# Optimization experiments

Measured on AMD Instinct MI355X. Metric: run time of the kernel, lower is better.

## Reference

```python
import jax, jax.numpy as jnp
import numpy as np

B, T, D = 4, 2048, 1024
DK, DV = 1024, 1024
BETA1, BETA2 = 1.0, 1.0
EPS = 1e-12  # torch F.normalize eps


def setup_inputs() -> dict:
    key = jax.random.key(0)
    kx, kq, kk, kv, ko = jax.random.split(key, 5)
    def w(k, shape):
        return jax.random.normal(k, shape, dtype=jnp.float32) * (shape[0] ** -0.5)
    return {
        "x": jax.random.normal(kx, (B, T, D), dtype=jnp.float32),
        # Weights stored [in, out]; torch Linear is x @ W.T with W [out, in] -- equivalent math.
        "Wq": w(kq, (D, DK)),
        "Wk": w(kk, (D, DK)),
        "Wv": w(kv, (D, DV)),
        "Wo": w(ko, (DV, D)),
    }


def reference(x, Wq, Wk, Wv, Wo):
    scale = DK ** -0.5
    q = (x @ Wq) * scale                      # [B,T,DK]
    k = x @ Wk
    k = k / jnp.maximum(jnp.linalg.norm(k, axis=-1, keepdims=True), EPS)
    v = x @ Wv                                # [B,T,DV]
    # time-major for scan
    qT = jnp.swapaxes(q, 0, 1)
    kT = jnp.swapaxes(k, 0, 1)
    vT = jnp.swapaxes(v, 0, 1)
    S0 = jnp.zeros((B, DV, DK), dtype=x.dtype)

    def step(S, qkv_t):
        q_t, k_t, v_t = qkv_t                 # each [B, d]
        # S @ (I - b1 k k^T) = S - b1 (S k) k^T   (same math, rank-1 form)
        Sk = jnp.einsum('bvk,bk->bv', S, k_t)
        S = S - BETA1 * Sk[:, :, None] * k_t[:, None, :] \
              + BETA2 * v_t[:, :, None] * k_t[:, None, :]
        o_t = jnp.einsum('bvk,bk->bv', S, q_t)
        return S, o_t

    _, oT = jax.lax.scan(step, S0, (qT, kT, vT))  # oT: [T,B,DV]
    out = jnp.swapaxes(oT, 0, 1) @ Wo             # [B,T,D]
    return out
```

## Files before the change

### kernel.cpp

```cpp
#include <hip/hip_runtime.h>

typedef unsigned short u16;
typedef __attribute__((ext_vector_type(8))) short short8;
typedef __attribute__((ext_vector_type(4))) float floatx4;

#define B_ 4
#define T_ 2048
#define CH 64

__device__ __forceinline__ u16 f2bf(float f) {
  unsigned int x = __float_as_uint(f);
  return (u16)((x + 0x7FFFu + ((x >> 16) & 1u)) >> 16);
}
__device__ __forceinline__ float bf2f(u16 u) {
  union { unsigned int i; float f; } v; v.i = ((unsigned int)u) << 16; return v.f;
}

__device__ __forceinline__ void barrier_lgkm() {
  asm volatile("s_waitcnt lgkmcnt(0)\n\ts_barrier" ::: "memory");
}

#define GL(dst, addr, IMM) \
  asm volatile("global_load_dwordx4 %0, %1, off offset:" #IMM : "=v"(dst) : "v"(addr))
#define GLU(dst, addr, IMM) \
  asm volatile("global_load_ushort %0, %1, off offset:" #IMM : "=v"(dst) : "v"(addr))
#define GS(addr, val, IMM) \
  asm volatile("global_store_short %0, %1, off offset:" #IMM :: "v"(addr), "v"(val))

#define GLA(slot, base, I0, I1, I2, I3) do { \
  GL(af[slot][0], base, I0); GL(af[slot][1], base, I1); \
  GL(af[slot][2], base, I2); GL(af[slot][3], base, I3); } while (0)

#define GLKT(nt0) do { \
  const u16* kp0_ = ktb + (size_t)(nt0) * ktstep; \
  GL(ktf[nt0][0], kp0_, 0); GL(ktf[nt0][1], kp0_, 64); \
  const u16* kp1_ = ktb + (size_t)(nt0 + 1) * ktstep; \
  GL(ktf[nt0 + 1][0], kp1_, 0); GL(ktf[nt0 + 1][1], kp1_, 64); } while (0)

#define GLX4 do { \
  GL(wpf0, wrow, 0); GL(wpf1, wrow, 64); \
  GLU(vv0, vvb, 0); GLU(vv1, vvb, 2048); \
  GLU(vv2, vvb2, 0); GLU(vv3, vvb2, 2048); } while (0)

#define NOOP ((void)0)

#define AITER(K, NW, PREFETCH, XCODE) do { \
  asm volatile("s_waitcnt vmcnt(" #NW ")"); \
  __builtin_amdgcn_sched_barrier(0x387); \
  PREFETCH; \
  XCODE; \
  short8 b0_ = *reinterpret_cast<const short8*>(&Sb[l16][(K * 4 + 0) * 32 + quad * 8]); \
  short8 b1_ = *reinterpret_cast<const short8*>(&Sb[l16][(K * 4 + 1) * 32 + quad * 8]); \
  short8 b2_ = *reinterpret_cast<const short8*>(&Sb[l16][(K * 4 + 2) * 32 + quad * 8]); \
  short8 b3_ = *reinterpret_cast<const short8*>(&Sb[l16][(K * 4 + 3) * 32 + quad * 8]); \
  ac0 = __builtin_amdgcn_mfma_f32_16x16x32_bf16(af[K][0], b0_, ac0, 0, 0, 0); \
  ac1 = __builtin_amdgcn_mfma_f32_16x16x32_bf16(af[K][1], b1_, ac1, 0, 0, 0); \
  ac2 = __builtin_amdgcn_mfma_f32_16x16x32_bf16(af[K][2], b2_, ac2, 0, 0, 0); \
  ac3 = __builtin_amdgcn_mfma_f32_16x16x32_bf16(af[K][3], b3_, ac3, 0, 0, 0); \
} while (0)

__global__ __launch_bounds__(256) void xconv_kernel(const float* __restrict__ x,
                                                    u16* __restrict__ Xbf) {
  size_t idx = ((size_t)blockIdx.x * 256 + threadIdx.x) * 4;
  float4 v = *reinterpret_cast<const float4*>(&x[idx]);
  ushort4 o;
  o.x = f2bf(v.x); o.y = f2bf(v.y); o.z = f2bf(v.z); o.w = f2bf(v.w);
  *reinterpret_cast<ushort4*>(&Xbf[idx]) = o;
}

__global__ __launch_bounds__(256) void wtrans_kernel(
    const float* __restrict__ W0, const float* __restrict__ W1,
    const float* __restrict__ W2, const float* __restrict__ W3,
    u16* __restrict__ T0, u16* __restrict__ T1,
    u16* __restrict__ T2, u16* __restrict__ T3)
{
  const int z = blockIdx.z;
  const float* W = (z == 0) ? W0 : (z == 1) ? W1 : (z == 2) ? W2 : W3;
  u16* T = (z == 0) ? T0 : (z == 1) ? T1 : (z == 2) ? T2 : T3;
  const int k0 = blockIdx.x * 64, n0 = blockIdx.y * 64;
  const int tid = threadIdx.x;
  __shared__ float Tile[64][65];
#pragma unroll
  for (int i = 0; i < 4; ++i) {
    int lin = tid + i * 256;
    int r = lin >> 4, c4 = (lin & 15) * 4;
    *reinterpret_cast<float4*>(&Tile[r][c4]) =
        *reinterpret_cast<const float4*>(&W[(size_t)(k0 + r) * 1024 + n0 + c4]);
  }
  __syncthreads();
#pragma unroll
  for (int i = 0; i < 4; ++i) {
    int lin = tid + i * 256;
    int r = lin >> 4, c4 = (lin & 15) * 4;
    ushort4 o;
    o.x = f2bf(Tile[c4 + 0][r]); o.y = f2bf(Tile[c4 + 1][r]);
    o.z = f2bf(Tile[c4 + 2][r]); o.w = f2bf(Tile[c4 + 3][r]);
    *reinterpret_cast<ushort4*>(&T[(size_t)(n0 + r) * 1024 + k0 + c4]) = o;
  }
}

__global__ __launch_bounds__(256) void mgemm_qkv(
    const u16* __restrict__ Xbf,
    const u16* __restrict__ WqT, const u16* __restrict__ WkT, const u16* __restrict__ WvT,
    u16* __restrict__ Qbf, u16* __restrict__ Kbf, u16* __restrict__ Vbf,
    int tg, int lsh)
{
  const int z = blockIdx.z;
  const u16* BT = (z == 0) ? WqT : ((z == 1) ? WkT : WvT);
  u16* O = (z == 0) ? Qbf : ((z == 1) ? Kbf : Vbf);
  const float scale = (z == 0) ? 0.03125f : 1.0f;
  const int r0 = blockIdx.x * 128, c0 = blockIdx.y * 128;
  const int tid = threadIdx.x;
  const int lane = tid & 63, wave = tid >> 6;
  const int quad = lane >> 4, l16 = lane & 15;
  const int wr = (wave >> 1) * 64, wc = (wave & 1) * 64;

  __shared__ u16 As[128][40];
  __shared__ u16 Bs[128][40];

  const int ar = tid >> 1, ac = (tid & 1) * 16;
  const int lr = r0 + ar;
  const int agrow = ((lr >> lsh) << 11) + tg + (lr & ((1 << lsh) - 1));
  const u16* aptr = &Xbf[(size_t)agrow * 1024 + ac];
  const u16* bptr = &BT[(size_t)(c0 + ar) * 1024 + ac];

  floatx4 acc[4][4] = {};
  for (int k0 = 0; k0 < 1024; k0 += 32) {
    float4 av0 = *reinterpret_cast<const float4*>(aptr + k0);
    float4 av1 = *reinterpret_cast<const float4*>(aptr + k0 + 8);
    float4 bv0 = *reinterpret_cast<const float4*>(bptr + k0);
    float4 bv1 = *reinterpret_cast<const float4*>(bptr + k0 + 8);
    __syncthreads();
    *reinterpret_cast<float4*>(&As[ar][ac]) = av0;
    *reinterpret_cast<float4*>(&As[ar][ac + 8]) = av1;
    *reinterpret_cast<float4*>(&Bs[ar][ac]) = bv0;
    *reinterpret_cast<float4*>(&Bs[ar][ac + 8]) = bv1;
    __syncthreads();
    short8 afr[4], bfr[4];
#pragma unroll
    for (int i = 0; i < 4; ++i) {
      afr[i] = *reinterpret_cast<const short8*>(&As[wr + i * 16 + l16][quad * 8]);
      bfr[i] = *reinterpret_cast<const short8*>(&Bs[wc + i * 16 + l16][quad * 8]);
    }
#pragma unroll
    for (int mi = 0; mi < 4; ++mi)
#pragma unroll
      for (int ni = 0; ni < 4; ++ni)
        acc[mi][ni] = __builtin_amdgcn_mfma_f32_16x16x32_bf16(afr[mi], bfr[ni], acc[mi][ni], 0, 0, 0);
  }
#pragma unroll
  for (int mi = 0; mi < 4; ++mi)
#pragma unroll
    for (int reg = 0; reg < 4; ++reg) {
      int row = r0 + wr + mi * 16 + quad * 4 + reg;
#pragma unroll
      for (int ni = 0; ni < 4; ++ni) {
        int col = c0 + wc + ni * 16 + l16;
        O[(size_t)row * 1024 + col] = f2bf(acc[mi][ni][reg] * scale);
      }
    }
}

__global__ __launch_bounds__(256) void mgemm_out(
    const u16* __restrict__ Obf, const u16* __restrict__ WoT,
    float* __restrict__ out, int tg, int lsh)
{
  const int r0 = blockIdx.x * 128, c0 = blockIdx.y * 128;
  const int tid = threadIdx.x;
  const int lane = tid & 63, wave = tid >> 6;
  const int quad = lane >> 4, l16 = lane & 15;
  const int wr = (wave >> 1) * 64, wc = (wave & 1) * 64;

  __shared__ u16 As[128][40];
  __shared__ u16 Bs[128][40];

  const int ar = tid >> 1, ac = (tid & 1) * 16;
  const u16* aptr = &Obf[(size_t)(r0 + ar) * 1024 + ac];
  const u16* bptr = &WoT[(size_t)(c0 + ar) * 1024 + ac];

  floatx4 acc[4][4] = {};
  for (int k0 = 0; k0 < 1024; k0 += 32) {
    float4 av0 = *reinterpret_cast<const float4*>(aptr + k0);
    float4 av1 = *reinterpret_cast<const float4*>(aptr + k0 + 8);
    float4 bv0 = *reinterpret_cast<const float4*>(bptr + k0);
    float4 bv1 = *reinterpret_cast<const float4*>(bptr + k0 + 8);
    __syncthreads();
    *reinterpret_cast<float4*>(&As[ar][ac]) = av0;
    *reinterpret_cast<float4*>(&As[ar][ac + 8]) = av1;
    *reinterpret_cast<float4*>(&Bs[ar][ac]) = bv0;
    *reinterpret_cast<float4*>(&Bs[ar][ac + 8]) = bv1;
    __syncthreads();
    short8 afr[4], bfr[4];
#pragma unroll
    for (int i = 0; i < 4; ++i) {
      afr[i] = *reinterpret_cast<const short8*>(&As[wr + i * 16 + l16][quad * 8]);
      bfr[i] = *reinterpret_cast<const short8*>(&Bs[wc + i * 16 + l16][quad * 8]);
    }
#pragma unroll
    for (int mi = 0; mi < 4; ++mi)
#pragma unroll
      for (int ni = 0; ni < 4; ++ni)
        acc[mi][ni] = __builtin_amdgcn_mfma_f32_16x16x32_bf16(afr[mi], bfr[ni], acc[mi][ni], 0, 0, 0);
  }
#pragma unroll
  for (int mi = 0; mi < 4; ++mi)
#pragma unroll
    for (int reg = 0; reg < 4; ++reg) {
      int lr = r0 + wr + mi * 16 + quad * 4 + reg;
      int grow = ((lr >> lsh) << 11) + tg + (lr & ((1 << lsh) - 1));
#pragma unroll
      for (int ni = 0; ni < 4; ++ni) {
        int col = c0 + wc + ni * 16 + l16;
        out[(size_t)grow * 1024 + col] = acc[mi][ni][reg];
      }
    }
}

__global__ __launch_bounds__(256) void knorm_kernel(u16* __restrict__ Kbf) {
  const int row = blockIdx.x;
  const int tid = threadIdx.x;
  ushort4 v4 = *reinterpret_cast<const ushort4*>(&Kbf[(size_t)row * 1024 + tid * 4]);
  float a = bf2f(v4.x), b = bf2f(v4.y), c = bf2f(v4.z), d = bf2f(v4.w);
  float ss = a * a + b * b + c * c + d * d;
#pragma unroll
  for (int off = 32; off > 0; off >>= 1) ss += __shfl_down(ss, off);
  __shared__ float wsum[4];
  if ((tid & 63) == 0) wsum[tid >> 6] = ss;
  __syncthreads();
  float tot = wsum[0] + wsum[1] + wsum[2] + wsum[3];
  float inv = 1.0f / fmaxf(sqrtf(tot), 1e-12f);
  ushort4 o;
  o.x = f2bf(a * inv); o.y = f2bf(b * inv); o.z = f2bf(c * inv); o.w = f2bf(d * inv);
  *reinterpret_cast<ushort4*>(&Kbf[(size_t)row * 1024 + tid * 4]) = o;
}

__global__ __launch_bounds__(256) void ktrans_kernel(const u16* __restrict__ Kbf,
                                                     u16* __restrict__ KT,
                                                     int tgs) {
  const int t0 = blockIdx.x * 64;
  const int d0 = blockIdx.y * 64;
  const int b = blockIdx.z;
  const int tid = threadIdx.x;
  __shared__ u16 Tile[64][68];
#pragma unroll
  for (int i = 0; i < 4; ++i) {
    int lin = tid + i * 256;
    int r = lin >> 4, c4 = (lin & 15) * 4;
    *reinterpret_cast<ushort4*>(&Tile[r][c4]) =
        *reinterpret_cast<const ushort4*>(&Kbf[(size_t)(b * tgs + t0 + r) * 1024 + d0 + c4]);
  }
  __syncthreads();
#pragma unroll
  for (int i = 0; i < 4; ++i) {
    int lin = tid + i * 256;
    int r = lin >> 4, c4 = (lin & 15) * 4;
    ushort4 o;
    o.x = Tile[c4 + 0][r]; o.y = Tile[c4 + 1][r];
    o.z = Tile[c4 + 2][r]; o.w = Tile[c4 + 3][r];
    *reinterpret_cast<ushort4*>(&KT[((size_t)b * 1024 + d0 + r) * tgs + t0 + c4]) = o;
  }
}

__global__ __launch_bounds__(256) void attn_winv_kernel(
    const u16* __restrict__ Qbf, const u16* __restrict__ Kbf,
    u16* __restrict__ Pb, u16* __restrict__ Wb, int tgs)
{
  const int cc = blockIdx.x;
  const int b = blockIdx.y;
  const int base = b * tgs + cc * CH;
  const int tid = threadIdx.x;
  const int lane = tid & 63;
  const int wave = tid >> 6;
  const int quad = lane >> 4, l16 = lane & 15;
  const int m0 = wave * 16;

  __shared__ float Asm[64][64];
  __shared__ float Wsm[64][65];

  floatx4 accA[4] = {};
  floatx4 accP[4] = {};
  const u16* arowK = &Kbf[(size_t)(base + m0 + l16) * 1024];
  const u16* arowQ = &Qbf[(size_t)(base + m0 + l16) * 1024];
#pragma unroll 4
  for (int kk = 0; kk < 32; ++kk) {
    short8 aK = *reinterpret_cast<const short8*>(&arowK[kk * 32 + quad * 8]);
    short8 aQ = *reinterpret_cast<const short8*>(&arowQ[kk * 32 + quad * 8]);
#pragma unroll
    for (int nt = 0; nt < 4; ++nt) {
      short8 bK = *reinterpret_cast<const short8*>(
          &Kbf[(size_t)(base + nt * 16 + l16) * 1024 + kk * 32 + quad * 8]);
      accA[nt] = __builtin_amdgcn_mfma_f32_16x16x32_bf16(aK, bK, accA[nt], 0, 0, 0);
      accP[nt] = __builtin_amdgcn_mfma_f32_16x16x32_bf16(aQ, bK, accP[nt], 0, 0, 0);
    }
  }
  const size_t pw0 = ((size_t)(cc * B_ + b) * CH) * 64;
#pragma unroll
  for (int nt = 0; nt < 4; ++nt) {
#pragma unroll
    for (int reg = 0; reg < 4; ++reg) {
      int t = m0 + quad * 4 + reg;
      int i = nt * 16 + l16;
      Asm[t][i] = (i < t) ? accA[nt][reg] : 0.0f;
      Pb[pw0 + (size_t)t * 64 + i] = f2bf((i <= t) ? accP[nt][reg] : 0.0f);
    }
  }
  __syncthreads();

  if (tid < 64) {
    const int j = tid;
    for (int t = 0; t < 64; ++t) {
      float s = (t == j) ? 1.0f : 0.0f;
      for (int i = 0; i < t; ++i) s -= Asm[t][i] * Wsm[i][j];
      Wsm[t][j] = s;
    }
    for (int t = 0; t < 64; ++t)
      Wb[pw0 + (size_t)t * 64 + j] = f2bf(Wsm[t][j]);
  }
}

__global__ __launch_bounds__(512, 2) void chain_kernel(
    const u16* __restrict__ Qbf, const u16* __restrict__ Kbf,
    const u16* __restrict__ KT, const u16* __restrict__ Vbf,
    u16* __restrict__ Obf, const u16* __restrict__ Wb, const u16* __restrict__ Pb,
    float* __restrict__ Sglob, int lsh, int cpg, int g, int ngrp)
{
  const int wg = blockIdx.x;
  const int t8 = wg & 7;
  const int b = t8 >> 1;
  const int sl = ((wg >> 3) << 1) | (t8 & 1);
  const int c0 = sl * 16;
  const int tgs = 1 << lsh;
  const int tid = threadIdx.x;
  const int lane = tid & 63;
  const int wave = tid >> 6;
  const int quad = lane >> 4, l16 = lane & 15;
  const int d0w = wave * 128;
  const bool isK = (wave < 4);
  const int m0 = (isK ? wave : (wave - 4)) * 16;
  const size_t ktstep = (size_t)16 * tgs;

  __shared__ u16 Sb[16][1048];
  __shared__ u16 rhsT[16][88];
  __shared__ u16 uT[16][88];

  floatx4 Sreg[8];
  if (g == 0) {
#pragma unroll
    for (int nt = 0; nt < 8; ++nt) Sreg[nt] = (floatx4){0.f, 0.f, 0.f, 0.f};
    for (int idx = tid; idx < 16 * 256; idx += 512) {
      int r = idx >> 8, d4 = (idx & 255) * 4;
      ushort4 z4 = {0, 0, 0, 0};
      *reinterpret_cast<ushort4*>(&Sb[r][d4]) = z4;
    }
  } else {
#pragma unroll
    for (int nt = 0; nt < 8; ++nt)
#pragma unroll
      for (int reg = 0; reg < 4; ++reg)
        Sreg[nt][reg] = Sglob[((size_t)b * 1024 + c0 + quad * 4 + reg) * 1024 +
                              d0w + nt * 16 + l16];
    for (int idx = tid; idx < 16 * 1024; idx += 512) {
      int r = idx >> 10, d = idx & 1023;
      Sb[r][d] = f2bf(Sglob[((size_t)b * 1024 + c0 + r) * 1024 + d]);
    }
  }
  __syncthreads();

  const u16* const Abase = isK ? Kbf : Qbf;
  const u16* arow = Abase + (size_t)(b * tgs + m0 + l16) * 1024;

  short8 af[8][4];
  short8 ktf[8][2];
  short8 wpf0, wpf1;
  unsigned int vv0, vv1, vv2, vv3;

  {
    const u16* aq0 = arow + quad * 8;
    GLA(0, aq0, 0, 64, 128, 192);
    GLA(1, aq0, 256, 320, 384, 448);
  }

  for (int cc = 0; cc < cpg; ++cc) {
    const int base = b * tgs + cc * CH;
    const size_t pw0 = ((size_t)(cc * B_ + b) * CH) * 64;

    const u16* aq   = arow + quad * 8;
    const u16* aqn  = arow + (size_t)(cc + 1 < cpg ? CH * 1024 : 0) + quad * 8;
    const u16* ktb  = KT + ((size_t)b * 1024 + d0w + l16) * tgs + (size_t)cc * CH + quad * 8;
    const u16* wrow = (isK ? Wb : Pb) + pw0 + (size_t)(m0 + l16) * 64 + quad * 8;
    const u16* vvb  = Vbf + (size_t)(base + m0 + quad * 4) * 1024 + c0 + l16;
    const u16* vvb2 = vvb + 2048;

    floatx4 ac0 = {}, ac1 = {}, ac2 = {}, ac3 = {};

    AITER(0, 4,  GLA(2, aq, 512, 576, 640, 704),     GLKT(0));
    AITER(1, 8,  GLA(3, aq, 768, 832, 896, 960),     GLKT(2));
    AITER(2, 12, GLA(4, aq, 1024, 1088, 1152, 1216), GLKT(4));
    AITER(3, 12, GLA(5, aq, 1280, 1344, 1408, 1472), GLKT(6));
    AITER(4, 12, GLA(6, aq, 1536, 1600, 1664, 1728), GLX4);
    AITER(5, 14, GLA(7, aq, 1792, 1856, 1920, 1984), NOOP);
    AITER(6, 10, GLA(0, aqn, 0, 64, 128, 192),       NOOP);
    AITER(7, 4,  GLA(1, aqn, 256, 320, 384, 448),    NOOP);

    asm volatile("s_waitcnt vmcnt(12)");
    __builtin_amdgcn_sched_barrier(0);

    floatx4 accS = (ac0 + ac1) + (ac2 + ac3);

    if (isK) {
      rhsT[l16][m0 + quad * 4 + 0] = f2bf(bf2f((u16)vv0) - accS[0]);
      rhsT[l16][m0 + quad * 4 + 1] = f2bf(bf2f((u16)vv1) - accS[1]);
      rhsT[l16][m0 + quad * 4 + 2] = f2bf(bf2f((u16)vv2) - accS[2]);
      rhsT[l16][m0 + quad * 4 + 3] = f2bf(bf2f((u16)vv3) - accS[3]);
    }
    barrier_lgkm();

    if (isK) {
      floatx4 uacc = {};
      short8 br0 = *reinterpret_cast<const short8*>(&rhsT[l16][quad * 8]);
      short8 br1 = *reinterpret_cast<const short8*>(&rhsT[l16][32 + quad * 8]);
      uacc = __builtin_amdgcn_mfma_f32_16x16x32_bf16(wpf0, br0, uacc, 0, 0, 0);
      uacc = __builtin_amdgcn_mfma_f32_16x16x32_bf16(wpf1, br1, uacc, 0, 0, 0);
#pragma unroll
      for (int reg = 0; reg < 4; ++reg)
        uT[l16][m0 + quad * 4 + reg] = f2bf(uacc[reg]);
    }
    barrier_lgkm();

    if (!isK) {
      floatx4 oacc = accS;
      short8 bu0 = *reinterpret_cast<const short8*>(&uT[l16][quad * 8]);
      short8 bu1 = *reinterpret_cast<const short8*>(&uT[l16][32 + quad * 8]);
      oacc = __builtin_amdgcn_mfma_f32_16x16x32_bf16(wpf0, bu0, oacc, 0, 0, 0);
      oacc = __builtin_amdgcn_mfma_f32_16x16x32_bf16(wpf1, bu1, oacc, 0, 0, 0);
      u16* ob  = Obf + (size_t)(base + m0 + quad * 4) * 1024 + c0 + l16;
      u16* ob2 = ob + 2048;
      unsigned int s0 = f2bf(oacc[0]), s1 = f2bf(oacc[1]);
      unsigned int s2 = f2bf(oacc[2]), s3 = f2bf(oacc[3]);
      GS(ob, s0, 0);  GS(ob, s1, 2048);
      GS(ob2, s2, 0); GS(ob2, s3, 2048);
    }

    {
      short8 ua0 = *reinterpret_cast<const short8*>(&uT[l16][quad * 8]);
      short8 ua1 = *reinterpret_cast<const short8*>(&uT[l16][32 + quad * 8]);
#pragma unroll
      for (int nt = 0; nt < 8; ++nt) {
        floatx4 cf = Sreg[nt];
        cf = __builtin_amdgcn_mfma_f32_16x16x32_bf16(ua0, ktf[nt][0], cf, 0, 0, 0);
        cf = __builtin_amdgcn_mfma_f32_16x16x32_bf16(ua1, ktf[nt][1], cf, 0, 0, 0);
        Sreg[nt] = cf;
        const int dn = d0w + nt * 16;
#pragma unroll
        for (int reg = 0; reg < 4; ++reg)
          Sb[quad * 4 + reg][dn + l16] = f2bf(cf[reg]);
      }
    }
    barrier_lgkm();
    arow += CH * 1024;
  }

  if (g < ngrp - 1) {
#pragma unroll
    for (int nt = 0; nt < 8; ++nt)
#pragma unroll
      for (int reg = 0; reg < 4; ++reg)
        Sglob[((size_t)b * 1024 + c0 + quad * 4 + reg) * 1024 + d0w + nt * 16 + l16] =
            Sreg[nt][reg];
  }
}

extern "C" void kernel_launch(void* const* d_in, const int* in_sizes, int n_in,
                              void* d_out, int out_size, void* d_ws, size_t ws_size,
                              hipStream_t stream) {
  const float* x  = (const float*)d_in[0];
  const float* Wq = (const float*)d_in[1];
  const float* Wk = (const float*)d_in[2];
  const float* Wv = (const float*)d_in[3];
  const float* Wo = (const float*)d_in[4];
  float* out = (float*)d_out;

  int lsh = 8;
  {
    const int cand[4] = {11, 10, 9, 8};
    for (int i = 0; i < 4; ++i) {
      size_t tgs = (size_t)1 << cand[i];
      size_t C = (size_t)B_ * tgs * 1024;
      size_t cpg = tgs / CH;
      size_t need = (size_t)B_ * T_ * 1024 * 2
                  + 4 * ((size_t)1024 * 1024 * 2)
                  + 5 * (C * 2)
                  + 2 * (cpg * B_ * CH * 64 * 2)
                  + (size_t)B_ * 1024 * 1024 * 4
                  + 32768;
      if (need <= ws_size) { lsh = cand[i]; break; }
    }
  }
  const int tgs = 1 << lsh;
  const int cpg = tgs / CH;
  const int ngrp = T_ / tgs;
  const int rows = B_ * tgs;

  char* ws = (char*)d_ws;
  size_t off = 0;
  auto alloc = [&](size_t bytes) -> void* {
    void* p = ws + off;
    off += (bytes + 255) & ~(size_t)255;
    return p;
  };
  u16* Xbf = (u16*)alloc((size_t)B_ * T_ * 1024 * 2);
  u16* WqT = (u16*)alloc((size_t)1024 * 1024 * 2);
  u16* WkT = (u16*)alloc((size_t)1024 * 1024 * 2);
  u16* WvT = (u16*)alloc((size_t)1024 * 1024 * 2);
  u16* WoT = (u16*)alloc((size_t)1024 * 1024 * 2);
  u16* Qbf = (u16*)alloc((size_t)rows * 1024 * 2);
  u16* Kbf = (u16*)alloc((size_t)rows * 1024 * 2);
  u16* Vbf = (u16*)alloc((size_t)rows * 1024 * 2);
  u16* KT  = (u16*)alloc((size_t)rows * 1024 * 2);
  u16* Obf = (u16*)alloc((size_t)rows * 1024 * 2);
  u16* Pb  = (u16*)alloc((size_t)cpg * B_ * CH * 64 * 2);
  u16* Wb  = (u16*)alloc((size_t)cpg * B_ * CH * 64 * 2);
  float* Sglob = (float*)alloc((size_t)B_ * 1024 * 1024 * 4);

  xconv_kernel<<<B_ * T_, 256, 0, stream>>>(x, Xbf);
  wtrans_kernel<<<dim3(16, 16, 4), 256, 0, stream>>>(Wq, Wk, Wv, Wo, WqT, WkT, WvT, WoT);

  for (int g = 0; g < ngrp; ++g) {
    int tg = g * tgs;
    mgemm_qkv<<<dim3(rows / 128, 8, 3), 256, 0, stream>>>(Xbf, WqT, WkT, WvT,
                                                          Qbf, Kbf, Vbf, tg, lsh);
    knorm_kernel<<<rows, 256, 0, stream>>>(Kbf);
    ktrans_kernel<<<dim3(tgs / 64, 16, B_), 256, 0, stream>>>(Kbf, KT, tgs);
    attn_winv_kernel<<<dim3(cpg, B_), 256, 0, stream>>>(Qbf, Kbf, Pb, Wb, tgs);
    chain_kernel<<<256, 512, 0, stream>>>(Qbf, Kbf, KT, Vbf, Obf, Wb, Pb, Sglob,
                                          lsh, cpg, g, ngrp);
    mgemm_out<<<dim3(rows / 128, 8), 256, 0, stream>>>(Obf, WoT, out, tg, lsh);
  }
}
```

Measured before the change: 628.1 us.

## Prefetch next chunk's K^T, W/P and V loads across loop iterations

```diff
diff --git a/kernel.cpp b/kernel.cpp
--- a/kernel.cpp
+++ b/kernel.cpp
@@ -32,23 +32,15 @@
   GL(af[slot][2], base, I2); GL(af[slot][3], base, I3); } while (0)
 
 #define GLKT(nt0) do { \
-  const u16* kp0_ = ktb + (size_t)(nt0) * ktstep; \
+  const u16* kp0_ = ktbn + (size_t)(nt0) * ktstep; \
   GL(ktf[nt0][0], kp0_, 0); GL(ktf[nt0][1], kp0_, 64); \
-  const u16* kp1_ = ktb + (size_t)(nt0 + 1) * ktstep; \
+  const u16* kp1_ = ktbn + (size_t)(nt0 + 1) * ktstep; \
   GL(ktf[nt0 + 1][0], kp1_, 0); GL(ktf[nt0 + 1][1], kp1_, 64); } while (0)
 
-#define GLX4 do { \
-  GL(wpf0, wrow, 0); GL(wpf1, wrow, 64); \
-  GLU(vv0, vvb, 0); GLU(vv1, vvb, 2048); \
-  GLU(vv2, vvb2, 0); GLU(vv3, vvb2, 2048); } while (0)
-
-#define NOOP ((void)0)
-
-#define AITER(K, NW, PREFETCH, XCODE) do { \
+#define A_IT(K, NW, PREFETCH) do { \
   asm volatile("s_waitcnt vmcnt(" #NW ")"); \
   __builtin_amdgcn_sched_barrier(0x387); \
   PREFETCH; \
-  XCODE; \
   short8 b0_ = *reinterpret_cast<const short8*>(&Sb[l16][(K * 4 + 0) * 32 + quad * 8]); \
   short8 b1_ = *reinterpret_cast<const short8*>(&Sb[l16][(K * 4 + 1) * 32 + quad * 8]); \
   short8 b2_ = *reinterpret_cast<const short8*>(&Sb[l16][(K * 4 + 2) * 32 + quad * 8]); \
@@ -367,43 +359,47 @@
   __syncthreads();
 
   const u16* const Abase = isK ? Kbf : Qbf;
-  const u16* arow = Abase + (size_t)(b * tgs + m0 + l16) * 1024;
+  const u16* const WPbase = isK ? Wb : Pb;
 
   short8 af[8][4];
   short8 ktf[8][2];
   short8 wpf0, wpf1;
   unsigned int vv0, vv1, vv2, vv3;
 
+  const u16* arow = Abase + (size_t)(b * tgs + m0 + l16) * 1024;
+
   {
     const u16* aq0 = arow + quad * 8;
     GLA(0, aq0, 0, 64, 128, 192);
     GLA(1, aq0, 256, 320, 384, 448);
+    const u16* ktbn = KT + ((size_t)b * 1024 + d0w + l16) * tgs + quad * 8;
+    GLKT(0); GLKT(2); GLKT(4); GLKT(6);
+    const u16* wrow0 = WPbase + (size_t)(b * CH * 0 + 0) + ((size_t)(0 * B_ + b) * CH) * 64 +
+                       (size_t)(m0 + l16) * 64 + quad * 8;
+    GL(wpf0, wrow0, 0); GL(wpf1, wrow0, 64);
+    const u16* vvb0  = Vbf + (size_t)(b * tgs + m0 + quad * 4) * 1024 + c0 + l16;
+    const u16* vvb02 = vvb0 + 2048;
+    GLU(vv0, vvb0, 0); GLU(vv1, vvb0, 2048);
+    GLU(vv2, vvb02, 0); GLU(vv3, vvb02, 2048);
   }
 
   for (int cc = 0; cc < cpg; ++cc) {
     const int base = b * tgs + cc * CH;
-    const size_t pw0 = ((size_t)(cc * B_ + b) * CH) * 64;
-
-    const u16* aq   = arow + quad * 8;
-    const u16* aqn  = arow + (size_t)(cc + 1 < cpg ? CH * 1024 : 0) + quad * 8;
-    const u16* ktb  = KT + ((size_t)b * 1024 + d0w + l16) * tgs + (size_t)cc * CH + quad * 8;
-    const u16* wrow = (isK ? Wb : Pb) + pw0 + (size_t)(m0 + l16) * 64 + quad * 8;
-    const u16* vvb  = Vbf + (size_t)(base + m0 + quad * 4) * 1024 + c0 + l16;
-    const u16* vvb2 = vvb + 2048;
+    const int nx = (cc + 1 < cpg) ? (cc + 1) : (cpg - 1);
+
+    const u16* aq  = arow + quad * 8;
+    const u16* aqn = arow + (size_t)(cc + 1 < cpg ? CH * 1024 : 0) + quad * 8;
 
     floatx4 ac0 = {}, ac1 = {}, ac2 = {}, ac3 = {};
 
-    AITER(0, 4,  GLA(2, aq, 512, 576, 640, 704),     GLKT(0));
-    AITER(1, 8,  GLA(3, aq, 768, 832, 896, 960),     GLKT(2));
-    AITER(2, 12, GLA(4, aq, 1024, 1088, 1152, 1216), GLKT(4));
-    AITER(3, 12, GLA(5, aq, 1280, 1344, 1408, 1472), GLKT(6));
-    AITER(4, 12, GLA(6, aq, 1536, 1600, 1664, 1728), GLX4);
-    AITER(5, 14, GLA(7, aq, 1792, 1856, 1920, 1984), NOOP);
-    AITER(6, 10, GLA(0, aqn, 0, 64, 128, 192),       NOOP);
-    AITER(7, 4,  GLA(1, aqn, 256, 320, 384, 448),    NOOP);
-
-    asm volatile("s_waitcnt vmcnt(12)");
-    __builtin_amdgcn_sched_barrier(0);
+    A_IT(0, 26, GLA(2, aq, 512, 576, 640, 704));
+    A_IT(1, 26, GLA(3, aq, 768, 832, 896, 960));
+    A_IT(2, 4,  GLA(4, aq, 1024, 1088, 1152, 1216));
+    A_IT(3, 4,  GLA(5, aq, 1280, 1344, 1408, 1472));
+    A_IT(4, 4,  GLA(6, aq, 1536, 1600, 1664, 1728));
+    A_IT(5, 4,  GLA(7, aq, 1792, 1856, 1920, 1984));
+    A_IT(6, 4,  GLA(0, aqn, 0, 64, 128, 192));
+    A_IT(7, 4,  GLA(1, aqn, 256, 320, 384, 448));
 
     floatx4 accS = (ac0 + ac1) + (ac2 + ac3);
 
@@ -427,12 +423,33 @@
     }
     barrier_lgkm();
 
+    short8 ua0 = *reinterpret_cast<const short8*>(&uT[l16][quad * 8]);
+    short8 ua1 = *reinterpret_cast<const short8*>(&uT[l16][32 + quad * 8]);
+
+    {
+#pragma unroll
+      for (int nt = 0; nt < 8; ++nt) {
+        floatx4 cf = Sreg[nt];
+        cf = __builtin_amdgcn_mfma_f32_16x16x32_bf16(ua0, ktf[nt][0], cf, 0, 0, 0);
+        cf = __builtin_amdgcn_mfma_f32_16x16x32_bf16(ua1, ktf[nt][1], cf, 0, 0, 0);
+        Sreg[nt] = cf;
+        const int dn = d0w + nt * 16;
+#pragma unroll
+        for (int reg = 0; reg < 4; ++reg)
+          Sb[quad * 4 + reg][dn + l16] = f2bf(cf[reg]);
+      }
+    }
+
+    {
+      const u16* ktbn = KT + ((size_t)b * 1024 + d0w + l16) * tgs +
+                        (size_t)nx * CH + quad * 8;
+      GLKT(0); GLKT(2); GLKT(4); GLKT(6);
+    }
+
     if (!isK) {
       floatx4 oacc = accS;
-      short8 bu0 = *reinterpret_cast<const short8*>(&uT[l16][quad * 8]);
-      short8 bu1 = *reinterpret_cast<const short8*>(&uT[l16][32 + quad * 8]);
-      oacc = __builtin_amdgcn_mfma_f32_16x16x32_bf16(wpf0, bu0, oacc, 0, 0, 0);
-      oacc = __builtin_amdgcn_mfma_f32_16x16x32_bf16(wpf1, bu1, oacc, 0, 0, 0);
+      oacc = __builtin_amdgcn_mfma_f32_16x16x32_bf16(wpf0, ua0, oacc, 0, 0, 0);
+      oacc = __builtin_amdgcn_mfma_f32_16x16x32_bf16(wpf1, ua1, oacc, 0, 0, 0);
       u16* ob  = Obf + (size_t)(base + m0 + quad * 4) * 1024 + c0 + l16;
       u16* ob2 = ob + 2048;
       unsigned int s0 = f2bf(oacc[0]), s1 = f2bf(oacc[1]);
@@ -442,23 +459,20 @@
     }
 
     {
-      short8 ua0 = *reinterpret_cast<const short8*>(&uT[l16][quad * 8]);
-      short8 ua1 = *reinterpret_cast<const short8*>(&uT[l16][32 + quad * 8]);
-#pragma unroll
-      for (int nt = 0; nt < 8; ++nt) {
-        floatx4 cf = Sreg[nt];
-        cf = __builtin_amdgcn_mfma_f32_16x16x32_bf16(ua0, ktf[nt][0], cf, 0, 0, 0);
-        cf = __builtin_amdgcn_mfma_f32_16x16x32_bf16(ua1, ktf[nt][1], cf, 0, 0, 0);
-        Sreg[nt] = cf;
-        const int dn = d0w + nt * 16;
-#pragma unroll
-        for (int reg = 0; reg < 4; ++reg)
-          Sb[quad * 4 + reg][dn + l16] = f2bf(cf[reg]);
-      }
-    }
+      const size_t pwN = ((size_t)(nx * B_ + b) * CH) * 64;
+      const u16* wrow = WPbase + pwN + (size_t)(m0 + l16) * 64 + quad * 8;
+      GL(wpf0, wrow, 0); GL(wpf1, wrow, 64);
+      const u16* vvb  = Vbf + (size_t)(b * tgs + nx * CH + m0 + quad * 4) * 1024 + c0 + l16;
+      const u16* vvb2 = vvb + 2048;
+      GLU(vv0, vvb, 0); GLU(vv1, vvb, 2048);
+      GLU(vv2, vvb2, 0); GLU(vv3, vvb2, 2048);
+    }
+
     barrier_lgkm();
     arow += CH * 1024;
   }
+
+  asm volatile("s_waitcnt vmcnt(0)");
 
   if (g < ngrp - 1) {
 #pragma unroll
```

After: 622.2 us. No clear change (-0.9%).
